# Performance work log

Hardware: AMD Instinct MI355X
Metric: run time of the kernel (lower is better)

Reference implementation:

```python
import jax, jax.numpy as jnp
import numpy as np

PS = 8  # window_size
LOCAL = 16  # split channels

def conv1x1(x, w, b):
    return jnp.einsum('oi,bihw->bohw', w, x) + b[None, :, None, None]

def dynamic_local(x, w1, b1, w2, b2, k):
    # x: (B, C, H, W); dynamic per-(batch,channel) depthwise conv with generated kernels
    B, C, H, W = x.shape
    pooled = x.mean((2, 3))                      # (B, C) adaptive avg pool to 1x1
    h = jax.nn.relu(pooled @ w1.T + b1)
    kern = (h @ w2.T + b2).reshape(B, C, k, k)   # per-sample depthwise kernels
    def per_batch(xb, kb):
        return jax.lax.conv_general_dilated(
            xb[None], kb[:, None], (1, 1), 'SAME',
            feature_group_count=C,
            dimension_numbers=('NCHW', 'OIHW', 'NCHW'))[0]
    return jax.vmap(per_batch)(x, kern)

def channel_layernorm(x, w, b, eps=1e-6):
    # LayerNorm over channel dim (torch module's non-channels_last path)
    u = x.mean(1, keepdims=True)
    s = ((x - u) ** 2).mean(1, keepdims=True)
    xn = (x - u) / jnp.sqrt(s + eps)
    return w[None, :, None, None] * xn + b[None, :, None, None]

def fsas(x, hid_w, hid_b, dw_w, dw_b, ln_w, ln_b, out_w, out_b):
    hidden = conv1x1(x, hid_w, hid_b)
    mid = hidden.shape[1]
    dw = jax.lax.conv_general_dilated(
        hidden, dw_w[:, None], (1, 1), 'SAME',
        feature_group_count=mid,
        dimension_numbers=('NCHW', 'OIHW', 'NCHW')) + dw_b[None, :, None, None]
    q, k, v = jnp.split(dw, 3, axis=1)
    B, C, H, W = q.shape
    def patch(t):
        # (B,C,H,W) -> (B,C,H/ps,W/ps,ps,ps)
        return t.reshape(B, C, H // PS, PS, W // PS, PS).transpose(0, 1, 2, 4, 3, 5)
    qf = jnp.fft.rfft2(patch(q))
    kf = jnp.fft.rfft2(patch(k))
    out = jnp.fft.irfft2(qf * kf, s=(PS, PS))
    out = out.transpose(0, 1, 2, 4, 3, 5).reshape(B, C, H, W)
    out = channel_layernorm(out, ln_w, ln_b)
    return conv1x1(v * out, out_w, out_b)


def setup_inputs() -> dict:
    key = jax.random.key(0)
    ks = jax.random.split(key, 12)
    s = 0.02
    return {
        'x': jax.random.normal(ks[0], (4, 64, 256, 256), jnp.float32),
        'dl1_w1': jax.random.normal(ks[1], (16, 16), jnp.float32) * s,
        'dl1_b1': jnp.zeros((16,), jnp.float32),
        'dl1_w2': jax.random.normal(ks[2], (144, 16), jnp.float32) * s,
        'dl1_b2': jnp.zeros((144,), jnp.float32),
        'dl2_w1': jax.random.normal(ks[3], (16, 16), jnp.float32) * s,
        'dl2_b1': jnp.zeros((16,), jnp.float32),
        'dl2_w2': jax.random.normal(ks[4], (400, 16), jnp.float32) * s,
        'dl2_b2': jnp.zeros((400,), jnp.float32),
        'fs_hid_w': jax.random.normal(ks[5], (144, 48), jnp.float32) * s,
        'fs_hid_b': jnp.zeros((144,), jnp.float32),
        'fs_dw_w': jax.random.normal(ks[6], (144, 3, 3), jnp.float32) * s,
        'fs_dw_b': jnp.zeros((144,), jnp.float32),
        'fs_ln_w': jnp.ones((48,), jnp.float32),
        'fs_ln_b': jnp.zeros((48,), jnp.float32),
        'fs_out_w': jax.random.normal(ks[7], (48, 48), jnp.float32) * s,
        'fs_out_b': jnp.zeros((48,), jnp.float32),
        'last_w': jax.random.normal(ks[8], (64, 64), jnp.float32) * s,
        'last_b': jnp.zeros((64,), jnp.float32),
    }


def reference(x, dl1_w1, dl1_b1, dl1_w2, dl1_b2, dl2_w1, dl2_b1, dl2_w2, dl2_b2,
              fs_hid_w, fs_hid_b, fs_dw_w, fs_dw_b, fs_ln_w, fs_ln_b,
              fs_out_w, fs_out_b, last_w, last_b):
    x1, x2 = x[:, :LOCAL], x[:, LOCAL:]
    x1 = dynamic_local(x1, dl1_w1, dl1_b1, dl1_w2, dl1_b2, 3)
    x1 = dynamic_local(x1, dl2_w1, dl2_b1, dl2_w2, dl2_b2, 5)
    x2 = fsas(x2, fs_hid_w, fs_hid_b, fs_dw_w, fs_dw_b, fs_ln_w, fs_ln_b, fs_out_w, fs_out_b)
    return conv1x1(jnp.concatenate([x1, x2], axis=1), last_w, last_b)
```

## Files before the change

### kernel.cpp

```cpp
#include <hip/hip_runtime.h>

typedef _Float16 h2 __attribute__((ext_vector_type(2)));
typedef _Float16 h4 __attribute__((ext_vector_type(4)));
typedef _Float16 h8 __attribute__((ext_vector_type(8)));
typedef float f4 __attribute__((ext_vector_type(4)));

#if defined(__has_builtin)
#if __has_builtin(__builtin_amdgcn_fdot2)
#define HAS_FDOT2 1
#endif
#endif

__device__ __forceinline__ float warpsum(float v) {
    for (int off = 32; off > 0; off >>= 1) v += __shfl_down(v, off);
    return v;
}

__device__ __forceinline__ int aswz(int p, int k) {
    return p * 72 + ((((k >> 3) ^ (p >> 3)) & 7) << 3) + (k & 7);
}
__device__ __forceinline__ int sswz(int p, int k) {
    return p * 64 + ((((k >> 3) ^ (p >> 3)) & 7) << 3) + (k & 7);
}

__global__ __launch_bounds__(256) void k_prep(const float* __restrict__ hid_w,
                                              const float* __restrict__ out_w,
                                              const float* __restrict__ last_w,
                                              _Float16* __restrict__ hwH,
                                              _Float16* __restrict__ owlwH) {
    int t = blockIdx.x * 256 + threadIdx.x;
    int stride = gridDim.x * 256;
    for (int i = t; i < 10368; i += stride) {
        int n = i / 72, k = i - n * 72;
        hwH[i] = (k < 48) ? (_Float16)hid_w[n * 48 + k] : (_Float16)0.f;
    }
    for (int i = t; i < 3456; i += stride) {
        int n = i / 72, k = i - n * 72;
        owlwH[i] = (k < 48) ? (_Float16)out_w[n * 48 + k] : (_Float16)0.f;
    }
    for (int i = t; i < 4608; i += stride) {
        int n = i / 72, k = i - n * 72;
        owlwH[3456 + i] = (k < 64) ? (_Float16)last_w[n * 64 + k] : (_Float16)0.f;
    }
}

__global__ __launch_bounds__(256) void k_pool(const float* __restrict__ x, float* __restrict__ pooled1) {
    int bid = blockIdx.x;
    int b = bid >> 4, c = bid & 15;
    const float* base = x + (size_t)(b * 64 + c) * 65536;
    float s = 0.f;
    for (int i = threadIdx.x; i < 16384; i += 256) {
        float4 v = ((const float4*)base)[i];
        s += v.x + v.y + v.z + v.w;
    }
    __shared__ float red[4];
    s = warpsum(s);
    if ((threadIdx.x & 63) == 0) red[threadIdx.x >> 6] = s;
    __syncthreads();
    if (threadIdx.x == 0) pooled1[bid] = (red[0] + red[1] + red[2] + red[3]) * (1.f / 65536.f);
}

__global__ __launch_bounds__(256) void k_kern1(const float* __restrict__ pooled1,
                                               const float* __restrict__ w1, const float* __restrict__ b1,
                                               const float* __restrict__ w2, const float* __restrict__ b2,
                                               float* __restrict__ kern1) {
    __shared__ float h[64];
    int t = threadIdx.x;
    if (t < 64) {
        int b = t >> 4, j = t & 15;
        float a = b1[j];
        for (int i = 0; i < 16; ++i) a += pooled1[b * 16 + i] * w1[j * 16 + i];
        h[t] = fmaxf(a, 0.f);
    }
    __syncthreads();
    for (int i = t; i < 576; i += 256) {
        int b = i / 144, o = i - b * 144;
        float a = b2[o];
        for (int j = 0; j < 16; ++j) a += h[b * 16 + j] * w2[o * 16 + j];
        kern1[i] = a;
    }
}

__global__ __launch_bounds__(256) void k_dw3(const float* __restrict__ x,
                                             const float* __restrict__ kern1,
                                             float* __restrict__ y1, float* __restrict__ rowsum) {
    __shared__ float tile[10][258];
    __shared__ float red[8][4];
    int bid = blockIdx.x;
    int rb = bid & 31, bc = bid >> 5;
    int b = bc >> 4, c = bc & 15;
    int row0 = rb << 3;
    int col = threadIdx.x;
    const float* xc = x + ((size_t)(b * 64 + c) << 16);
#pragma unroll
    for (int j = 0; j < 10; ++j) {
        int r = row0 - 1 + j;
        tile[j][col + 1] = ((unsigned)r < 256u) ? xc[(r << 8) + col] : 0.f;
    }
    if (col < 10) { tile[col][0] = 0.f; tile[col][257] = 0.f; }
    const float* k9 = kern1 + b * 144 + c * 9;
    float kk[9];
#pragma unroll
    for (int i = 0; i < 9; ++i) kk[i] = k9[i];
    __syncthreads();
#pragma unroll
    for (int j = 0; j < 8; ++j) {
        float acc = 0.f;
#pragma unroll
        for (int dy = 0; dy < 3; ++dy)
#pragma unroll
            for (int dx = 0; dx < 3; ++dx)
                acc += kk[dy * 3 + dx] * tile[j + dy][col + dx];
        y1[((size_t)bc << 16) + ((row0 + j) << 8) + col] = acc;
        float s = warpsum(acc);
        if ((col & 63) == 0) red[j][col >> 6] = s;
    }
    __syncthreads();
    if (col < 8) rowsum[bc * 256 + row0 + col] = red[col][0] + red[col][1] + red[col][2] + red[col][3];
}

__global__ __launch_bounds__(256) void k_kern2(const float* __restrict__ rowsum,
                                               const float* __restrict__ w1, const float* __restrict__ b1,
                                               const float* __restrict__ w2, const float* __restrict__ b2,
                                               float* __restrict__ kern2) {
    __shared__ float ps[256];
    __shared__ float p2[64];
    __shared__ float h[64];
    int t = threadIdx.x;
    {
        int pair = t >> 2, seg = t & 3;
        const float* rs = rowsum + pair * 256 + seg * 64;
        float s = 0.f;
        for (int j = 0; j < 64; ++j) s += rs[j];
        ps[t] = s;
    }
    __syncthreads();
    if (t < 64) p2[t] = (ps[t * 4] + ps[t * 4 + 1] + ps[t * 4 + 2] + ps[t * 4 + 3]) * (1.f / 65536.f);
    __syncthreads();
    if (t < 64) {
        int b = t >> 4, j = t & 15;
        float a = b1[j];
        for (int i = 0; i < 16; ++i) a += p2[b * 16 + i] * w1[j * 16 + i];
        h[t] = fmaxf(a, 0.f);
    }
    __syncthreads();
    for (int i = t; i < 1600; i += 256) {
        int b = i / 400, o = i - b * 400;
        float a = b2[o];
        for (int j = 0; j < 16; ++j) a += h[b * 16 + j] * w2[o * 16 + j];
        kern2[i] = a;
    }
}

__global__ __launch_bounds__(256) void k_dw5(const float* __restrict__ y1,
                                             const float* __restrict__ kern2,
                                             float* __restrict__ x1o) {
    __shared__ float tile[12][260];
    int bid = blockIdx.x;
    int rb = bid & 31, bc = bid >> 5;
    int b = bc >> 4, c = bc & 15;
    int row0 = rb << 3;
    int col = threadIdx.x;
    const float* yc = y1 + ((size_t)bc << 16);
#pragma unroll
    for (int j = 0; j < 12; ++j) {
        int r = row0 - 2 + j;
        tile[j][col + 2] = ((unsigned)r < 256u) ? yc[(r << 8) + col] : 0.f;
    }
    if (col < 12) { tile[col][0] = 0.f; tile[col][1] = 0.f; tile[col][258] = 0.f; tile[col][259] = 0.f; }
    const float* k25 = kern2 + b * 400 + c * 25;
    float kk[25];
#pragma unroll
    for (int i = 0; i < 25; ++i) kk[i] = k25[i];
    __syncthreads();
#pragma unroll
    for (int j = 0; j < 8; ++j) {
        float acc = 0.f;
#pragma unroll
        for (int dy = 0; dy < 5; ++dy)
#pragma unroll
            for (int dx = 0; dx < 5; ++dx)
                acc += kk[dy * 5 + dx] * tile[j + dy][col + dx];
        x1o[((size_t)bc << 16) + ((row0 + j) << 8) + col] = acc;
    }
}

__global__ __launch_bounds__(512, 8) void k_fsas(const float* __restrict__ x,
                                                 const _Float16* __restrict__ hwH, const float* __restrict__ hid_b,
                                                 const float* __restrict__ dw_w, const float* __restrict__ dw_b,
                                                 const float* __restrict__ ln_w, const float* __restrict__ ln_b,
                                                 const _Float16* __restrict__ owlwH, const float* __restrict__ out_b,
                                                 const float* __restrict__ last_b,
                                                 const float* __restrict__ x1o, float* __restrict__ out) {
    __shared__ __align__(16) _Float16 Abuf[9824];
    __shared__ __align__(16) _Float16 qbuf[3072];
    __shared__ __align__(16) _Float16 kbuf2[6528];
    __shared__ __align__(16) float pstat[128];

    _Float16* hbuf  = Abuf;
    _Float16* fbuf  = Abuf;
    float*    lnp   = (float*)(Abuf + 4608);
    _Float16* outb  = Abuf + 6656;
    _Float16* sbufA = kbuf2;

    int tid = threadIdx.x;
    int lane = tid & 63;
    int wave = __builtin_amdgcn_readfirstlane(tid >> 6);
    int bid = blockIdx.x;
    int swz = ((bid & 7) << 9) | (bid >> 3);
    int b = swz >> 10;
    int rem = swz & 1023;
    int row0 = (rem >> 5) << 3, col0 = (rem & 31) << 3;

    int l16 = lane & 15, lhi = lane >> 4;
    int mb = wave * 16 + (lhi << 2);
    bool st[4], vok[4];
#pragma unroll
    for (int r = 0; r < 4; ++r) {
        int m = mb + r;
        st[r] = (m < 120);
        int yv = m / 12, xv = m - yv * 12;
        vok[r] = st[r] && (xv < 10) &&
                 ((unsigned)(row0 - 1 + yv) < 256u) && ((unsigned)(col0 - 1 + xv) < 256u);
    }

    for (int j = tid; j < 5760; j += 512) {
        int k = j / 120, p = j - k * 120;
        int yv = p / 12, xv = p - yv * 12;
        int gy = row0 - 1 + yv, gx = col0 - 1 + xv;
        float v = 0.f;
        if (xv < 10 && (unsigned)gy < 256u && (unsigned)gx < 256u)
            v = x[((size_t)(b * 64 + 16 + k) << 16) + (gy << 8) + gx];
        Abuf[aswz(p, k)] = (_Float16)v;
    }
    for (int j = tid; j < 2048; j += 512) {
        int p = j >> 4, k = 48 + (j & 15);
        Abuf[aswz(p, k)] = (_Float16)0.f;
    }
    if (tid < 384) {
        int p = 120 + (tid / 48), k = tid % 48;
        Abuf[aswz(p, k)] = (_Float16)0.f;
    }
    __syncthreads();

    int arow = wave * 16 + l16;
    h8 a0 = *(const h8*)(Abuf + aswz(arow, lhi << 3));
    h8 a1 = *(const h8*)(Abuf + aswz(arow, 32 + (lhi << 3)));
    __syncthreads();

    int px2 = lane, pr = wave;
    size_t gpix2 = ((size_t)(row0 + (px2 >> 3)) << 8) + col0 + (px2 & 7);
    float xa = x1o[((size_t)(b * 16 + 2 * pr) << 16) + gpix2];
    float xb = x1o[((size_t)(b * 16 + 2 * pr + 1) << 16) + gpix2];

    int dch = tid >> 3, drow = tid & 7;
    h8 vreg;

#pragma unroll 1
    for (int ph = 0; ph < 3; ++ph) {
        const _Float16* wp = hwH + ph * 3456;
#pragma unroll 1
        for (int nt = 0; nt < 3; ++nt) {
            h8 b0 = *(const h8*)(wp + nt * 1152 + l16 * 72 + (lhi << 3));
            h8 b1 = *(const h8*)(wp + nt * 1152 + l16 * 72 + 32 + (lhi << 3));
            float bias = hid_b[ph * 48 + nt * 16 + l16];
            f4 acc = {bias, bias, bias, bias};
            acc = __builtin_amdgcn_mfma_f32_16x16x32_f16(a0, b0, acc, 0, 0, 0);
            acc = __builtin_amdgcn_mfma_f32_16x16x32_f16(a1, b1, acc, 0, 0, 0);
            int n_l = nt * 16 + l16;
#pragma unroll
            for (int r = 0; r < 4; ++r)
                if (st[r]) hbuf[n_l * 120 + mb + r] = vok[r] ? (_Float16)acc[r] : (_Float16)0.f;
        }
        __syncthreads();
        if (tid < 384) {
            int c = ph * 48 + dch;
            const float* dwp = dw_w + c * 9;
            float bias = dw_b[c];
            float o[8];
#pragma unroll
            for (int xx = 0; xx < 8; ++xx) o[xx] = bias;
            const _Float16* hb = hbuf + dch * 120 + drow * 12;
#pragma unroll
            for (int dy = 0; dy < 3; ++dy) {
                h4 r0 = *(const h4*)(hb + dy * 12);
                h4 r1 = *(const h4*)(hb + dy * 12 + 4);
                h2 r2 = *(const h2*)(hb + dy * 12 + 8);
                float rowv[10] = {(float)r0[0], (float)r0[1], (float)r0[2], (float)r0[3],
                                  (float)r1[0], (float)r1[1], (float)r1[2], (float)r1[3],
                                  (float)r2[0], (float)r2[1]};
                float w0 = dwp[dy * 3], w1 = dwp[dy * 3 + 1], w2 = dwp[dy * 3 + 2];
#pragma unroll
                for (int xx = 0; xx < 8; ++xx)
                    o[xx] += w0 * rowv[xx] + w1 * rowv[xx + 1] + w2 * rowv[xx + 2];
            }
            if (ph == 0) {
                h8 qv;
#pragma unroll
                for (int xx = 0; xx < 8; ++xx) qv[xx] = (_Float16)o[xx];
                *(h8*)(qbuf + dch * 64 + drow * 8) = qv;
            } else if (ph == 1) {
                h8 kr, ko;
#pragma unroll
                for (int t2 = 0; t2 < 8; ++t2) {
                    kr[t2] = (_Float16)o[(8 - t2) & 7];
                    ko[t2] = (_Float16)o[(9 - t2) & 7];
                }
                *(h8*)(kbuf2 + dch * 136 + drow * 16) = kr;
                *(h8*)(kbuf2 + dch * 136 + drow * 16 + 8) = ko;
            } else {
#pragma unroll
                for (int xx = 0; xx < 8; ++xx) vreg[xx] = (_Float16)o[xx];
            }
        }
        __syncthreads();
    }

    *(h2*)(fbuf + aswz(px2, 2 * pr)) = (h2){(_Float16)xa, (_Float16)xb};

    float co[8];
    if (tid < 384) {
        int ch = dch, m = drow;
#pragma unroll
        for (int n = 0; n < 8; ++n) co[n] = 0.f;
#pragma unroll
        for (int i8 = 0; i8 < 8; ++i8) {
            int r = (m - i8) & 7;
            h8 q8 = *(const h8*)(qbuf + ch * 64 + i8 * 8);
            h8 e8 = *(const h8*)(kbuf2 + ch * 136 + r * 16);
#ifdef HAS_FDOT2
            h8 o8 = *(const h8*)(kbuf2 + ch * 136 + r * 16 + 8);
            h2 qp[4], ep[4], op[4];
            qp[0] = __builtin_shufflevector(q8, q8, 0, 1); qp[1] = __builtin_shufflevector(q8, q8, 2, 3);
            qp[2] = __builtin_shufflevector(q8, q8, 4, 5); qp[3] = __builtin_shufflevector(q8, q8, 6, 7);
            ep[0] = __builtin_shufflevector(e8, e8, 0, 1); ep[1] = __builtin_shufflevector(e8, e8, 2, 3);
            ep[2] = __builtin_shufflevector(e8, e8, 4, 5); ep[3] = __builtin_shufflevector(e8, e8, 6, 7);
            op[0] = __builtin_shufflevector(o8, o8, 0, 1); op[1] = __builtin_shufflevector(o8, o8, 2, 3);
            op[2] = __builtin_shufflevector(o8, o8, 4, 5); op[3] = __builtin_shufflevector(o8, o8, 6, 7);
#pragma unroll
            for (int u = 0; u < 4; ++u)
#pragma unroll
                for (int a = 0; a < 4; ++a) {
                    co[2 * u]     = __builtin_amdgcn_fdot2(qp[a], ep[(a - u) & 3], co[2 * u], false);
                    co[2 * u + 1] = __builtin_amdgcn_fdot2(qp[a], op[(a - u) & 3], co[2 * u + 1], false);
                }
#else
            float qf[8], kf[8];
#pragma unroll
            for (int j = 0; j < 8; ++j) { qf[j] = (float)q8[j]; kf[j] = (float)e8[(8 - j) & 7]; }
#pragma unroll
            for (int j = 0; j < 8; ++j)
#pragma unroll
                for (int n = 0; n < 8; ++n)
                    co[n] += qf[j] * kf[(n - j) & 7];
#endif
        }
#pragma unroll
        for (int v = 0; v < 4; ++v)
            *(h2*)(outb + dch * 66 + drow * 8 + 2 * v) = (h2){(_Float16)co[2 * v], (_Float16)co[2 * v + 1]};
    }
    __syncthreads();

    {
        int px = tid & 63, g = tid >> 6;
        float s = 0.f, ss = 0.f;
#pragma unroll
        for (int cc = 0; cc < 6; ++cc) {
            float v = (float)outb[(g * 6 + cc) * 66 + px];
            s += v; ss += v * v;
        }
        lnp[g * 64 + px] = s;
        lnp[512 + g * 64 + px] = ss;
    }
    __syncthreads();
    if (tid < 64) {
        float s = 0.f, ss = 0.f;
#pragma unroll
        for (int g = 0; g < 8; ++g) { s += lnp[g * 64 + tid]; ss += lnp[512 + g * 64 + tid]; }
        float mu = s * (1.f / 48.f);
        float var = ss * (1.f / 48.f) - mu * mu;
        pstat[tid * 2] = mu;
        pstat[tid * 2 + 1] = rsqrtf(var + 1e-6f);
    }
    __syncthreads();

    if (tid < 384) {
        int ch = dch, m = drow;
        float lw = ln_w[ch], lb = ln_b[ch];
        const float* ps = pstat + m * 16;
#pragma unroll
        for (int n = 0; n < 8; ++n) {
            float mu = ps[2 * n], inv = ps[2 * n + 1];
            float lnv = lw * ((co[n] - mu) * inv) + lb;
            sbufA[sswz(m * 8 + n, ch)] = (_Float16)((float)vreg[n] * lnv);
        }
    }
    *(h2*)(sbufA + sswz(px2, 48 + ((tid >> 6) << 1))) = (h2){(_Float16)0.f, (_Float16)0.f};
    __syncthreads();

    for (int t = wave; t < 12; t += 8) {
        int mt = t / 3, nt = t - mt * 3;
        int row5 = mt * 16 + l16;
        h8 c0 = *(const h8*)(sbufA + sswz(row5, lhi << 3));
        h8 c1 = *(const h8*)(sbufA + sswz(row5, 32 + (lhi << 3)));
        h8 d0 = *(const h8*)(owlwH + nt * 1152 + l16 * 72 + (lhi << 3));
        h8 d1 = *(const h8*)(owlwH + nt * 1152 + l16 * 72 + 32 + (lhi << 3));
        float bias = out_b[nt * 16 + l16];
        f4 acc = {bias, bias, bias, bias};
        acc = __builtin_amdgcn_mfma_f32_16x16x32_f16(c0, d0, acc, 0, 0, 0);
        acc = __builtin_amdgcn_mfma_f32_16x16x32_f16(c1, d1, acc, 0, 0, 0);
        int n5 = nt * 16 + l16;
        int pb = mt * 16 + (lhi << 2);
#pragma unroll
        for (int r = 0; r < 4; ++r)
            fbuf[aswz(pb + r, 16 + n5)] = (_Float16)acc[r];
    }
    __syncthreads();

    for (int t = wave; t < 16; t += 8) {
        int mt = t >> 2, nt = t & 3;
        int row6 = mt * 16 + l16;
        h8 c0 = *(const h8*)(fbuf + aswz(row6, lhi << 3));
        h8 c1 = *(const h8*)(fbuf + aswz(row6, 32 + (lhi << 3)));
        h8 d0 = *(const h8*)(owlwH + 3456 + nt * 1152 + l16 * 72 + (lhi << 3));
        h8 d1 = *(const h8*)(owlwH + 3456 + nt * 1152 + l16 * 72 + 32 + (lhi << 3));
        float bias = last_b[nt * 16 + l16];
        f4 acc = {bias, bias, bias, bias};
        acc = __builtin_amdgcn_mfma_f32_16x16x32_f16(c0, d0, acc, 0, 0, 0);
        acc = __builtin_amdgcn_mfma_f32_16x16x32_f16(c1, d1, acc, 0, 0, 0);
        int ch = nt * 16 + l16;
        int px0 = mt * 16 + (lhi << 2);
        float4 val = {acc[0], acc[1], acc[2], acc[3]};
        *(float4*)(out + ((size_t)(b * 64 + ch) << 16) + ((size_t)(row0 + (px0 >> 3)) << 8) + col0 + (px0 & 7)) = val;
    }
}

extern "C" void kernel_launch(void* const* d_in, const int* in_sizes, int n_in,
                              void* d_out, int out_size, void* d_ws, size_t ws_size,
                              hipStream_t stream) {
    const float* x      = (const float*)d_in[0];
    const float* dl1_w1 = (const float*)d_in[1];
    const float* dl1_b1 = (const float*)d_in[2];
    const float* dl1_w2 = (const float*)d_in[3];
    const float* dl1_b2 = (const float*)d_in[4];
    const float* dl2_w1 = (const float*)d_in[5];
    const float* dl2_b1 = (const float*)d_in[6];
    const float* dl2_w2 = (const float*)d_in[7];
    const float* dl2_b2 = (const float*)d_in[8];
    const float* hid_w  = (const float*)d_in[9];
    const float* hid_b  = (const float*)d_in[10];
    const float* dw_w   = (const float*)d_in[11];
    const float* dw_b   = (const float*)d_in[12];
    const float* ln_w   = (const float*)d_in[13];
    const float* ln_b   = (const float*)d_in[14];
    const float* out_w  = (const float*)d_in[15];
    const float* out_b  = (const float*)d_in[16];
    const float* last_w = (const float*)d_in[17];
    const float* last_b = (const float*)d_in[18];
    float* out = (float*)d_out;

    float* ws      = (float*)d_ws;
    float* pooled1 = ws;
    float* kern1   = ws + 64;
    float* rowsum  = ws + 1024;
    float* kern2   = ws + 17408;
    _Float16* hwH   = (_Float16*)(ws + 19008);
    _Float16* owlwH = (_Float16*)(ws + 24192);
    float* y1      = ws + 32768;
    float* x1o     = ws + 32768 + 4194304;

    k_prep <<<8,    256, 0, stream>>>(hid_w, out_w, last_w, hwH, owlwH);
    k_pool <<<64,   256, 0, stream>>>(x, pooled1);
    k_kern1<<<1,    256, 0, stream>>>(pooled1, dl1_w1, dl1_b1, dl1_w2, dl1_b2, kern1);
    k_dw3  <<<2048, 256, 0, stream>>>(x, kern1, y1, rowsum);
    k_kern2<<<1,    256, 0, stream>>>(rowsum, dl2_w1, dl2_b1, dl2_w2, dl2_b2, kern2);
    k_dw5  <<<2048, 256, 0, stream>>>(y1, kern2, x1o);
    k_fsas <<<4096, 512, 0, stream>>>(x, hwH, hid_b, dw_w, dw_b, ln_w, ln_b,
                                      owlwH, out_b, last_b, x1o, out);
}
```

Baseline: 176.8 us.

## Compute all hidden channels in one pass with prefetched weights, fewer barriers

Replaces the three-phase hidden-conv/depthwise loop with a single pass. All nine weight tiles and biases are preloaded into registers, the full 144-channel hidden tensor is written to a larger shared buffer, and the depthwise work for all channels is spread across threads with only one barrier. The input staging is restructured so each thread loads whole 10-wide rows, padding is zeroed with vector stores, and the x1o loads are issued early by waves 6-7 and written later. The extra shared memory and registers mean launch bounds drop to 4 blocks, which lowers occupancy in exchange for fewer syncs and better load overlap.

Result: faster. 167.1 us (-5.5%).

```diff
diff --git a/kernel.cpp b/kernel.cpp
--- a/kernel.cpp
+++ b/kernel.cpp
@@ -185,22 +185,24 @@
     }
 }
 
-__global__ __launch_bounds__(512, 8) void k_fsas(const float* __restrict__ x,
+__global__ __launch_bounds__(512, 4) void k_fsas(const float* __restrict__ x,
                                                  const _Float16* __restrict__ hwH, const float* __restrict__ hid_b,
                                                  const float* __restrict__ dw_w, const float* __restrict__ dw_b,
                                                  const float* __restrict__ ln_w, const float* __restrict__ ln_b,
                                                  const _Float16* __restrict__ owlwH, const float* __restrict__ out_b,
                                                  const float* __restrict__ last_b,
                                                  const float* __restrict__ x1o, float* __restrict__ out) {
-    __shared__ __align__(16) _Float16 Abuf[9824];
+    __shared__ __align__(16) _Float16 Sbig[17856];
+    __shared__ __align__(16) _Float16 vbuf[3456];
     __shared__ __align__(16) _Float16 qbuf[3072];
     __shared__ __align__(16) _Float16 kbuf2[6528];
     __shared__ __align__(16) float pstat[128];
 
-    _Float16* hbuf  = Abuf;
-    _Float16* fbuf  = Abuf;
-    float*    lnp   = (float*)(Abuf + 4608);
-    _Float16* outb  = Abuf + 6656;
+    _Float16* Abuf  = Sbig;
+    _Float16* hbuf  = Sbig;
+    _Float16* fbuf  = Sbig;
+    float*    lnp   = (float*)(Sbig + 4608);
+    _Float16* outb  = Sbig + 6656;
     _Float16* sbufA = kbuf2;
 
     int tid = threadIdx.x;
@@ -224,22 +226,45 @@
                  ((unsigned)(row0 - 1 + yv) < 256u) && ((unsigned)(col0 - 1 + xv) < 256u);
     }
 
-    for (int j = tid; j < 5760; j += 512) {
-        int k = j / 120, p = j - k * 120;
-        int yv = p / 12, xv = p - yv * 12;
-        int gy = row0 - 1 + yv, gx = col0 - 1 + xv;
-        float v = 0.f;
-        if (xv < 10 && (unsigned)gy < 256u && (unsigned)gx < 256u)
-            v = x[((size_t)(b * 64 + 16 + k) << 16) + (gy << 8) + gx];
-        Abuf[aswz(p, k)] = (_Float16)v;
-    }
-    for (int j = tid; j < 2048; j += 512) {
-        int p = j >> 4, k = 48 + (j & 15);
-        Abuf[aswz(p, k)] = (_Float16)0.f;
-    }
-    if (tid < 384) {
-        int p = 120 + (tid / 48), k = tid % 48;
-        Abuf[aswz(p, k)] = (_Float16)0.f;
+    h8 wb0[9], wb1[9];
+    float biasr[9];
+#pragma unroll
+    for (int nt = 0; nt < 9; ++nt) {
+        const _Float16* wr = hwH + (nt * 16 + l16) * 72 + (lhi << 3);
+        wb0[nt] = *(const h8*)(wr);
+        wb1[nt] = *(const h8*)(wr + 32);
+        biasr[nt] = hid_b[nt * 16 + l16];
+    }
+    float xr[8];
+    int fpx = lane, fgrp = wave - 6;
+    if (wave >= 6) {
+        size_t gp = ((size_t)(row0 + (fpx >> 3)) << 8) + col0 + (fpx & 7);
+#pragma unroll
+        for (int j = 0; j < 8; ++j)
+            xr[j] = x1o[((size_t)(b * 16 + fgrp * 8 + j) << 16) + gp];
+    }
+
+    if (tid < 480) {
+        int k = tid / 10, y = tid - (tid / 10) * 10;
+        int gy = row0 - 1 + y;
+        bool rowok = (unsigned)gy < 256u;
+        const float* xk = x + ((size_t)(b * 64 + 16 + k) << 16) + ((size_t)(gy & 255) << 8);
+#pragma unroll
+        for (int xx = 0; xx < 10; ++xx) {
+            int gx = col0 - 1 + xx;
+            float v = (rowok && (unsigned)gx < 256u) ? xk[gx] : 0.f;
+            Abuf[aswz(y * 12 + xx, k)] = (_Float16)v;
+        }
+        Abuf[aswz(y * 12 + 10, k)] = (_Float16)0.f;
+        Abuf[aswz(y * 12 + 11, k)] = (_Float16)0.f;
+    }
+    if (tid < 256) {
+        int p = tid >> 1, kb = 48 + ((tid & 1) << 3);
+        *(h8*)(Abuf + aswz(p, kb)) = (h8)(_Float16)0.f;
+    }
+    if (tid < 48) {
+        int p = 120 + tid / 6, kb = (tid % 6) << 3;
+        *(h8*)(Abuf + aswz(p, kb)) = (h8)(_Float16)0.f;
     }
     __syncthreads();
 
@@ -248,39 +273,28 @@
     h8 a1 = *(const h8*)(Abuf + aswz(arow, 32 + (lhi << 3)));
     __syncthreads();
 
-    int px2 = lane, pr = wave;
-    size_t gpix2 = ((size_t)(row0 + (px2 >> 3)) << 8) + col0 + (px2 & 7);
-    float xa = x1o[((size_t)(b * 16 + 2 * pr) << 16) + gpix2];
-    float xb = x1o[((size_t)(b * 16 + 2 * pr + 1) << 16) + gpix2];
-
-    int dch = tid >> 3, drow = tid & 7;
-    h8 vreg;
-
-#pragma unroll 1
-    for (int ph = 0; ph < 3; ++ph) {
-        const _Float16* wp = hwH + ph * 3456;
-#pragma unroll 1
-        for (int nt = 0; nt < 3; ++nt) {
-            h8 b0 = *(const h8*)(wp + nt * 1152 + l16 * 72 + (lhi << 3));
-            h8 b1 = *(const h8*)(wp + nt * 1152 + l16 * 72 + 32 + (lhi << 3));
-            float bias = hid_b[ph * 48 + nt * 16 + l16];
-            f4 acc = {bias, bias, bias, bias};
-            acc = __builtin_amdgcn_mfma_f32_16x16x32_f16(a0, b0, acc, 0, 0, 0);
-            acc = __builtin_amdgcn_mfma_f32_16x16x32_f16(a1, b1, acc, 0, 0, 0);
-            int n_l = nt * 16 + l16;
-#pragma unroll
-            for (int r = 0; r < 4; ++r)
-                if (st[r]) hbuf[n_l * 120 + mb + r] = vok[r] ? (_Float16)acc[r] : (_Float16)0.f;
-        }
-        __syncthreads();
-        if (tid < 384) {
-            int c = ph * 48 + dch;
-            const float* dwp = dw_w + c * 9;
-            float bias = dw_b[c];
+#pragma unroll
+    for (int nt = 0; nt < 9; ++nt) {
+        float bias = biasr[nt];
+        f4 acc = {bias, bias, bias, bias};
+        acc = __builtin_amdgcn_mfma_f32_16x16x32_f16(a0, wb0[nt], acc, 0, 0, 0);
+        acc = __builtin_amdgcn_mfma_f32_16x16x32_f16(a1, wb1[nt], acc, 0, 0, 0);
+        int n_l = nt * 16 + l16;
+#pragma unroll
+        for (int r = 0; r < 4; ++r)
+            if (st[r]) hbuf[n_l * 124 + mb + r] = vok[r] ? (_Float16)acc[r] : (_Float16)0.f;
+    }
+    __syncthreads();
+
+    {
+        int row = tid & 7;
+        auto dw_task = [&](int ch) {
+            const float* dwp = dw_w + ch * 9;
             float o[8];
+            float bias = dw_b[ch];
 #pragma unroll
             for (int xx = 0; xx < 8; ++xx) o[xx] = bias;
-            const _Float16* hb = hbuf + dch * 120 + drow * 12;
+            const _Float16* hb = hbuf + ch * 124 + row * 12;
 #pragma unroll
             for (int dy = 0; dy < 3; ++dy) {
                 h4 r0 = *(const h4*)(hb + dy * 12);
@@ -294,31 +308,37 @@
                 for (int xx = 0; xx < 8; ++xx)
                     o[xx] += w0 * rowv[xx] + w1 * rowv[xx + 1] + w2 * rowv[xx + 2];
             }
-            if (ph == 0) {
+            if (ch < 48) {
                 h8 qv;
 #pragma unroll
                 for (int xx = 0; xx < 8; ++xx) qv[xx] = (_Float16)o[xx];
-                *(h8*)(qbuf + dch * 64 + drow * 8) = qv;
-            } else if (ph == 1) {
+                *(h8*)(qbuf + ch * 64 + row * 8) = qv;
+            } else if (ch < 96) {
+                int kc = ch - 48;
                 h8 kr, ko;
 #pragma unroll
                 for (int t2 = 0; t2 < 8; ++t2) {
                     kr[t2] = (_Float16)o[(8 - t2) & 7];
                     ko[t2] = (_Float16)o[(9 - t2) & 7];
                 }
-                *(h8*)(kbuf2 + dch * 136 + drow * 16) = kr;
-                *(h8*)(kbuf2 + dch * 136 + drow * 16 + 8) = ko;
+                *(h8*)(kbuf2 + kc * 136 + row * 16) = kr;
+                *(h8*)(kbuf2 + kc * 136 + row * 16 + 8) = ko;
             } else {
-#pragma unroll
-                for (int xx = 0; xx < 8; ++xx) vreg[xx] = (_Float16)o[xx];
+                int vc = ch - 96;
+                h8 vv;
+#pragma unroll
+                for (int xx = 0; xx < 8; ++xx) vv[xx] = (_Float16)o[xx];
+                *(h8*)(vbuf + vc * 72 + row * 8) = vv;
             }
-        }
-        __syncthreads();
-    }
-
-    *(h2*)(fbuf + aswz(px2, 2 * pr)) = (h2){(_Float16)xa, (_Float16)xb};
+        };
+        dw_task(tid >> 3);
+        dw_task(64 + (tid >> 3));
+        if (tid < 128) dw_task(128 + (tid >> 3));
+    }
+    __syncthreads();
 
     float co[8];
+    int dch = tid >> 3, drow = tid & 7;
     if (tid < 384) {
         int ch = dch, m = drow;
 #pragma unroll
@@ -358,6 +378,11 @@
 #pragma unroll
         for (int v = 0; v < 4; ++v)
             *(h2*)(outb + dch * 66 + drow * 8 + 2 * v) = (h2){(_Float16)co[2 * v], (_Float16)co[2 * v + 1]};
+    } else {
+        h8 fv;
+#pragma unroll
+        for (int j = 0; j < 8; ++j) fv[j] = (_Float16)xr[j];
+        *(h8*)(fbuf + aswz(fpx, fgrp * 8)) = fv;
     }
     __syncthreads();
 
@@ -387,15 +412,16 @@
     if (tid < 384) {
         int ch = dch, m = drow;
         float lw = ln_w[ch], lb = ln_b[ch];
+        h8 vv = *(const h8*)(vbuf + ch * 72 + m * 8);
         const float* ps = pstat + m * 16;
 #pragma unroll
         for (int n = 0; n < 8; ++n) {
             float mu = ps[2 * n], inv = ps[2 * n + 1];
             float lnv = lw * ((co[n] - mu) * inv) + lb;
-            sbufA[sswz(m * 8 + n, ch)] = (_Float16)((float)vreg[n] * lnv);
+            sbufA[sswz(m * 8 + n, ch)] = (_Float16)((float)vv[n] * lnv);
         }
     }
-    *(h2*)(sbufA + sswz(px2, 48 + ((tid >> 6) << 1))) = (h2){(_Float16)0.f, (_Float16)0.f};
+    *(h2*)(sbufA + sswz(lane, 48 + (wave << 1))) = (h2){(_Float16)0.f, (_Float16)0.f};
     __syncthreads();
 
     for (int t = wave; t < 12; t += 8) {
```
